# Kernel optimization log

Measured on AMD Instinct MI355X. Metric: run time of the kernel, lower is better.

## Reference

```python
import jax, jax.numpy as jnp
import numpy as np

B, L, DIM = 16, 1024, 768
HEADS, DIM_HEAD = 12, 64
INNER = HEADS * DIM_HEAD  # 768


def _make_perm(key, l, dim):
    # first `dim` entries identity, rest a random permutation of [dim, l*dim)
    tail = dim + jax.random.permutation(key, (l - 1) * dim)
    return jnp.concatenate([jnp.arange(dim), tail]).astype(jnp.int32)


def setup_inputs() -> dict:
    key = jax.random.key(0)
    kx, kq, kk, kv, ko, kp1, kp2 = jax.random.split(key, 7)
    s = DIM ** -0.5
    return {
        "x": jax.random.normal(kx, (B, L, DIM), dtype=jnp.float32),
        "Wq": jax.random.normal(kq, (DIM, INNER), dtype=jnp.float32) * s,
        "Wk": jax.random.normal(kk, (DIM, INNER), dtype=jnp.float32) * s,
        "Wv": jax.random.normal(kv, (DIM, INNER), dtype=jnp.float32) * s,
        "Wo": jax.random.normal(ko, (INNER, DIM), dtype=jnp.float32) * (INNER ** -0.5),
        "bo": jnp.zeros((DIM,), dtype=jnp.float32),
        "permq": _make_perm(kp1, L, DIM),
        "permk": _make_perm(kp2, L, DIM),
    }


def reference(x, Wq, Wk, Wv, Wo, bo, permq, permk):
    b, l, d = x.shape
    scale = DIM_HEAD ** -0.5
    flat = x.reshape(b, l * d)
    xq = flat[:, permq].reshape(b, l, d)  # irregular gather across (seq*dim)
    xk = flat[:, permk].reshape(b, l, d)
    # projections + head split: b n (h d) -> b h n d
    q = (xq @ Wq).reshape(b, l, HEADS, DIM_HEAD).transpose(0, 2, 1, 3)
    k = (xk @ Wk).reshape(b, l, HEADS, DIM_HEAD).transpose(0, 2, 1, 3)
    v = (x @ Wv).reshape(b, l, HEADS, DIM_HEAD).transpose(0, 2, 1, 3)
    dots = jnp.einsum('bhnd,bhmd->bhnm', q, k) * scale
    attn = jax.nn.softmax(dots, axis=-1)
    out = jnp.einsum('bhnm,bhmd->bhnd', attn, v)
    out = out.transpose(0, 2, 1, 3).reshape(b, l, INNER)
    return out @ Wo + bo
```

## Files before the change

kernel.cpp:

```cpp
#include <hip/hip_runtime.h>

typedef unsigned short u16;
typedef __attribute__((ext_vector_type(8))) short bf16x8;
typedef __attribute__((ext_vector_type(4))) float f32x4;
typedef __attribute__((ext_vector_type(16))) float f32x16;

#define MFMA16(a, b, c) __builtin_amdgcn_mfma_f32_16x16x32_bf16(a, b, c, 0, 0, 0)
#define MFMA32(a, b, c) __builtin_amdgcn_mfma_f32_32x32x16_bf16(a, b, c, 0, 0, 0)

#if defined(__has_builtin)
# if __has_builtin(__builtin_amdgcn_cvt_pk_bf16_f32)
#  define HAS_CVT_PK 1
# else
#  define HAS_CVT_PK 0
# endif
#else
# define HAS_CVT_PK 0
#endif

__device__ __forceinline__ u16 f2b(float f) {
    union { float f; unsigned int u; } v;
    v.f = f;
    unsigned int u = v.u;
    return (u16)((u + 0x7fffu + ((u >> 16) & 1u)) >> 16);
}

__device__ __forceinline__ unsigned int f2b_pk(float a, float b) {
#if HAS_CVT_PK
    auto r = __builtin_amdgcn_cvt_pk_bf16_f32(a, b);
    unsigned int u;
    __builtin_memcpy(&u, &r, 4);
    return u;
#else
    return (unsigned int)f2b(a) | ((unsigned int)f2b(b) << 16);
#endif
}

__device__ __forceinline__ unsigned int cvtpk_asm(float a, float b) {
    unsigned int r;
    asm("v_cvt_pk_bf16_f32 %0, %1, %2" : "=v"(r) : "v"(a), "v"(b));
    return r;
}

__device__ __forceinline__ void g2l16(const u16* gsrc, u16* ldst) {
    __builtin_amdgcn_global_load_lds(
        (const __attribute__((address_space(1))) void*)gsrc,
        (__attribute__((address_space(3))) void*)ldst,
        16, 0, 0);
}

__global__ __launch_bounds__(256) void prep_weights(
    const float* __restrict__ Wq, const float* __restrict__ Wk,
    const float* __restrict__ Wv, const float* __restrict__ Wo,
    u16* __restrict__ wqt, u16* __restrict__ wkt,
    u16* __restrict__ wvt, u16* __restrict__ wot) {
    int id = blockIdx.x * 256 + threadIdx.x;
    int k = id / 768, n = id % 768;
    int t = n * 768 + k;
    wqt[t] = f2b(Wq[id] * (0.125f * 1.44269504088896340736f));
    wkt[t] = f2b(Wk[id]);
    wvt[t] = f2b(Wv[id]);
    wot[t] = f2b(Wo[id]);
}

__global__ __launch_bounds__(256) void cast_transpose(
    const float* __restrict__ x, u16* __restrict__ xb, u16* __restrict__ xT) {
    __shared__ __attribute__((aligned(16))) u16 T[16 * 1032];
    int t = threadIdx.x;
    int j0 = blockIdx.x * 1024;
#pragma unroll
    for (int b = 0; b < 16; ++b) {
        float4 v = *(const float4*)&x[(size_t)b * 786432 + j0 + 4 * t];
        uint2 o = make_uint2(f2b_pk(v.x, v.y), f2b_pk(v.z, v.w));
        *(uint2*)&T[b * 1032 + 4 * t] = o;
        *(uint2*)&xb[(size_t)b * 786432 + j0 + 4 * t] = o;
    }
    __syncthreads();
#pragma unroll
    for (int p = 0; p < 4; ++p) {
        int jl = t + 256 * p;
        union { u16 u[16]; int4 v[2]; } r;
#pragma unroll
        for (int b = 0; b < 16; ++b) r.u[b] = T[b * 1032 + jl];
        size_t base = (size_t)(j0 + jl) * 16;
        *(int4*)&xT[base] = r.v[0];
        *(int4*)&xT[base + 8] = r.v[1];
    }
}

__global__ __launch_bounds__(256) void gather_rows(
    const u16* __restrict__ xT, const int* __restrict__ permq,
    const int* __restrict__ permk, u16* __restrict__ xqT,
    u16* __restrict__ xkT) {
    int j = blockIdx.x * 256 + threadIdx.x;
    int pq = permq[j], pk = permk[j];
    const int4* sq = (const int4*)&xT[(size_t)pq * 16];
    const int4* sk = (const int4*)&xT[(size_t)pk * 16];
    int4 q0 = sq[0], q1 = sq[1];
    int4 k0 = sk[0], k1 = sk[1];
    int4* dq = (int4*)&xqT[(size_t)j * 16];
    int4* dk = (int4*)&xkT[(size_t)j * 16];
    dq[0] = q0; dq[1] = q1;
    dk[0] = k0; dk[1] = k1;
}

__global__ __launch_bounds__(256) void untranspose(
    const u16* __restrict__ srcQ, const u16* __restrict__ srcK,
    u16* __restrict__ dstQ, u16* __restrict__ dstK) {
    __shared__ u16 T[16 * 1034];
    const u16* src = blockIdx.y ? srcK : srcQ;
    u16* dst = blockIdx.y ? dstK : dstQ;
    int t = threadIdx.x;
    int j0 = blockIdx.x * 1024;
#pragma unroll
    for (int p = 0; p < 8; ++p) {
        int c = p * 256 + t;
        union { u16 u[8]; int4 v; } r;
        r.v = *(const int4*)&src[(size_t)j0 * 16 + c * 8];
        int jl = c >> 1, h = (c & 1) * 8;
#pragma unroll
        for (int w = 0; w < 8; ++w) T[(h + w) * 1034 + jl] = r.u[w];
    }
    __syncthreads();
#pragma unroll
    for (int b = 0; b < 16; ++b) {
        const unsigned int* s = (const unsigned int*)&T[b * 1034 + 4 * t];
        uint2 o = make_uint2(s[0], s[1]);
        *(uint2*)&dst[(size_t)b * 786432 + j0 + 4 * t] = o;
    }
}

__device__ __forceinline__ void gemm_core(
    const u16* __restrict__ A, const u16* __restrict__ Bt,
    u16* __restrict__ Cb, float* __restrict__ Cf,
    const float* __restrict__ bias, int M, int K, int N, int mode) {
    __shared__ __attribute__((aligned(16))) u16 As[128 * 32];
    __shared__ __attribute__((aligned(16))) u16 Bs[128 * 32];
    int tid = threadIdx.x;
    int m0 = blockIdx.y * 128, n0 = blockIdx.x * 128;
    int wave = tid >> 6, lane = tid & 63;
    int lo = lane & 15, quad = lane >> 4;
    int wm = (wave >> 1) * 64, wn = (wave & 1) * 64;
    f32x4 acc[4][4] = {};

    int c0 = wave * 64 + lane;
    int c1 = 256 + c0;
    const u16* pA0 = A + (size_t)(m0 + (c0 >> 2)) * K + (c0 & 3) * 8;
    const u16* pA1 = A + (size_t)(m0 + (c1 >> 2)) * K + (c1 & 3) * 8;
    const u16* pB0 = Bt + (size_t)(n0 + (c0 >> 2)) * K + (c0 & 3) * 8;
    const u16* pB1 = Bt + (size_t)(n0 + (c1 >> 2)) * K + (c1 & 3) * 8;
    u16* lA0 = &As[(wave * 64) * 8];
    u16* lA1 = &As[(256 + wave * 64) * 8];
    u16* lB0 = &Bs[(wave * 64) * 8];
    u16* lB1 = &Bs[(256 + wave * 64) * 8];

    for (int k0 = 0; k0 < K; k0 += 32) {
        __syncthreads();
        g2l16(pA0, lA0); g2l16(pA1, lA1);
        g2l16(pB0, lB0); g2l16(pB1, lB1);
        pA0 += 32; pA1 += 32; pB0 += 32; pB1 += 32;
        __syncthreads();
        bf16x8 af[4], bf[4];
#pragma unroll
        for (int mi = 0; mi < 4; ++mi)
            af[mi] = *(const bf16x8*)&As[(wm + mi * 16 + lo) * 32 + quad * 8];
#pragma unroll
        for (int nj = 0; nj < 4; ++nj)
            bf[nj] = *(const bf16x8*)&Bs[(wn + nj * 16 + lo) * 32 + quad * 8];
#pragma unroll
        for (int mi = 0; mi < 4; ++mi)
#pragma unroll
            for (int nj = 0; nj < 4; ++nj)
                acc[mi][nj] = MFMA16(af[mi], bf[nj], acc[mi][nj]);
    }
#pragma unroll
    for (int mi = 0; mi < 4; ++mi)
#pragma unroll
        for (int nj = 0; nj < 4; ++nj) {
            int col = n0 + wn + nj * 16 + lo;
#pragma unroll
            for (int r = 0; r < 4; ++r) {
                int row = m0 + wm + mi * 16 + quad * 4 + r;
                float v = acc[mi][nj][r];
                if (mode) Cf[(size_t)row * N + col] = v + bias[col];
                else      Cb[(size_t)row * N + col] = f2b(v);
            }
        }
}

__global__ __launch_bounds__(256) void gemm_qkv(
    const u16* __restrict__ xqb, const u16* __restrict__ wqt, u16* __restrict__ Qb,
    const u16* __restrict__ xkb, const u16* __restrict__ wkt, u16* __restrict__ Kb,
    const u16* __restrict__ xb,  const u16* __restrict__ wvt, u16* __restrict__ Vb) {
    int z = blockIdx.z;
    const u16* A = (z == 0) ? xqb : (z == 1) ? xkb : xb;
    const u16* W = (z == 0) ? wqt : (z == 1) ? wkt : wvt;
    u16* C = (z == 0) ? Qb : (z == 1) ? Kb : Vb;
    gemm_core(A, W, C, nullptr, nullptr, 16384, 768, 768, 0);
}

__global__ __launch_bounds__(256) void gemm_out(
    const u16* __restrict__ A, const u16* __restrict__ Bt,
    float* __restrict__ Cf, const float* __restrict__ bias) {
    gemm_core(A, Bt, nullptr, Cf, bias, 16384, 768, 768, 1);
}

#define LDA 72
__global__ __launch_bounds__(256) void transpose_v(
    const u16* __restrict__ Vb, u16* __restrict__ Vt) {
    __shared__ __attribute__((aligned(16))) u16 tile[64 * LDA];
    int lt = blockIdx.x;
    int bh = blockIdx.y;
    int b = bh / 12, h = bh % 12;
    int tid = threadIdx.x;
    int row = tid >> 3, co = (tid & 7) * 8;
#pragma unroll
    for (int p = 0; p < 2; ++p) {
        int r2 = row + p * 32;
        *(int4*)&tile[r2 * LDA + co] =
            *(const int4*)&Vb[(size_t)(b * 1024 + lt * 64 + r2) * 768 + h * 64 + co];
    }
    __syncthreads();
    int d = tid >> 2, nc = (tid & 3) * 16;
    union { u16 u[16]; int4 v[2]; } tt;
#pragma unroll
    for (int j = 0; j < 16; ++j)
        tt.u[j] = tile[(nc + j) * LDA + d];
    size_t base = ((size_t)bh * 64 + d) * 1024 + lt * 64 + nc;
    *(int4*)&Vt[base] = tt.v[0];
    *(int4*)&Vt[base + 8] = tt.v[1];
}

#define LDK 72
__global__ __launch_bounds__(256) void flash_attn(
    const u16* __restrict__ Qb, const u16* __restrict__ Kb,
    const u16* __restrict__ Vt, u16* __restrict__ AO) {
    __shared__ __attribute__((aligned(16))) u16 Ks[64 * LDK];
    __shared__ __attribute__((aligned(16))) u16 Vs[64 * LDK];
    int id = blockIdx.x;
    int bh = (id & 7) + ((id >> 6) << 3);
    int qt = (id >> 3) & 7;
    int b = bh / 12, h = bh % 12;
    int tid = threadIdx.x, wave = tid >> 6, lane = tid & 63;
    int ln = lane & 31, hi = lane >> 5;
    int q0 = qt * 128;

    bf16x8 qa[4];
    {
        const u16* qrow = &Qb[(size_t)(b * 1024 + q0 + wave * 32 + ln) * 768 + h * 64 + hi * 8];
#pragma unroll
        for (int kk = 0; kk < 4; ++kk)
            qa[kk] = *(const bf16x8*)&qrow[kk * 16];
    }

    const float M2 = 24.0f;
    float l_own = 0.0f;
    f32x16 acc_o[2] = {};
    const size_t kbase = (size_t)b * 1024 * 768 + h * 64;
    const size_t vbase = (size_t)bh * 64 * 1024;
    int srow = tid >> 3, sco = (tid & 7) * 8;

    int4 kr0 = *(const int4*)&Kb[kbase + (size_t)srow * 768 + sco];
    int4 kr1 = *(const int4*)&Kb[kbase + (size_t)(srow + 32) * 768 + sco];
    int4 vr0 = *(const int4*)&Vt[vbase + (size_t)srow * 1024 + sco];
    int4 vr1 = *(const int4*)&Vt[vbase + (size_t)(srow + 32) * 1024 + sco];

    for (int t = 0; t < 16; ++t) {
        __syncthreads();
        *(int4*)&Ks[srow * LDK + sco] = kr0;
        *(int4*)&Ks[(srow + 32) * LDK + sco] = kr1;
        *(int4*)&Vs[srow * LDK + sco] = vr0;
        *(int4*)&Vs[(srow + 32) * LDK + sco] = vr1;
        __syncthreads();
        int tn = (t + 1) & 15;
        kr0 = *(const int4*)&Kb[kbase + (size_t)(tn * 64 + srow) * 768 + sco];
        kr1 = *(const int4*)&Kb[kbase + (size_t)(tn * 64 + srow + 32) * 768 + sco];
        vr0 = *(const int4*)&Vt[vbase + (size_t)srow * 1024 + tn * 64 + sco];
        vr1 = *(const int4*)&Vt[vbase + (size_t)(srow + 32) * 1024 + tn * 64 + sco];
        f32x16 sacc[2] = {};
#pragma unroll
        for (int nj = 0; nj < 2; ++nj)
#pragma unroll
            for (int kk = 0; kk < 4; ++kk) {
                bf16x8 kb = *(const bf16x8*)&Ks[(ln + 32 * nj) * LDK + kk * 16 + hi * 8];
                sacc[nj] = MFMA32(kb, qa[kk], sacc[nj]);
            }
#pragma unroll
        for (int nj = 0; nj < 2; ++nj) {
            float p[16];
#pragma unroll
            for (int r = 0; r < 16; ++r)
                p[r] = __builtin_amdgcn_exp2f(sacc[nj][r] - M2);
            l_own += (((p[0] + p[1]) + (p[2] + p[3])) + ((p[4] + p[5]) + (p[6] + p[7])))
                   + (((p[8] + p[9]) + (p[10] + p[11])) + ((p[12] + p[13]) + (p[14] + p[15])));
            unsigned int c[8];
#pragma unroll
            for (int m = 0; m < 8; ++m)
                c[m] = cvtpk_asm(p[2 * m], p[2 * m + 1]);
            asm("v_permlane32_swap_b32 %0, %1" : "+v"(c[0]), "+v"(c[2]));
            asm("v_permlane32_swap_b32 %0, %1" : "+v"(c[1]), "+v"(c[3]));
            asm("v_permlane32_swap_b32 %0, %1" : "+v"(c[4]), "+v"(c[6]));
            asm("v_permlane32_swap_b32 %0, %1" : "+v"(c[5]), "+v"(c[7]));
            union { unsigned int w[4]; bf16x8 v; } pa0, pa1;
            pa0.w[0] = c[0]; pa0.w[1] = c[1]; pa0.w[2] = c[2]; pa0.w[3] = c[3];
            pa1.w[0] = c[4]; pa1.w[1] = c[5]; pa1.w[2] = c[6]; pa1.w[3] = c[7];
#pragma unroll
            for (int njd = 0; njd < 2; ++njd) {
                bf16x8 vb0 = *(const bf16x8*)&Vs[(ln + 32 * njd) * LDK + (2 * nj) * 16 + hi * 8];
                acc_o[njd] = MFMA32(pa0.v, vb0, acc_o[njd]);
            }
#pragma unroll
            for (int njd = 0; njd < 2; ++njd) {
                bf16x8 vb1 = *(const bf16x8*)&Vs[(ln + 32 * njd) * LDK + (2 * nj + 1) * 16 + hi * 8];
                acc_o[njd] = MFMA32(pa1.v, vb1, acc_o[njd]);
            }
        }
    }
    float l = l_own + __shfl_xor(l_own, 32, 64);
    float inv = 1.0f / l;
#pragma unroll
    for (int r = 0; r < 16; ++r) {
        int qrow = (r & 3) + 8 * (r >> 2) + 4 * hi;
        float invq = __shfl(inv, qrow, 64);
        int row = b * 1024 + q0 + wave * 32 + qrow;
#pragma unroll
        for (int njd = 0; njd < 2; ++njd)
            AO[(size_t)row * 768 + h * 64 + ln + 32 * njd] = f2b(acc_o[njd][r] * invq);
    }
}

static const size_t SZ_W  = (size_t)768 * 768 * 2;
static const size_t SZ_X  = (size_t)16 * 1024 * 768 * 2;
static const size_t OFF_WQT = 0;
static const size_t OFF_WKT = SZ_W;
static const size_t OFF_WVT = 2 * SZ_W;
static const size_t OFF_WOT = 3 * SZ_W;
static const size_t OFF_XB  = 4 * SZ_W;
static const size_t OFF_XQB = OFF_XB  + SZ_X;
static const size_t OFF_XKB = OFF_XQB + SZ_X;
static const size_t OFF_QB  = OFF_XKB + SZ_X;
static const size_t OFF_KB  = OFF_QB  + SZ_X;
static const size_t OFF_VB  = OFF_KB  + SZ_X;
static const size_t OFF_XT  = OFF_QB;
static const size_t OFF_XQT = OFF_KB;
static const size_t OFF_XKT = OFF_VB;
static const size_t OFF_VT  = OFF_XQB;
static const size_t OFF_AO  = OFF_XKB;

extern "C" void kernel_launch(void* const* d_in, const int* in_sizes, int n_in,
                              void* d_out, int out_size, void* d_ws, size_t ws_size,
                              hipStream_t stream) {
    const float* x  = (const float*)d_in[0];
    const float* Wq = (const float*)d_in[1];
    const float* Wk = (const float*)d_in[2];
    const float* Wv = (const float*)d_in[3];
    const float* Wo = (const float*)d_in[4];
    const float* bo = (const float*)d_in[5];
    const int* permq = (const int*)d_in[6];
    const int* permk = (const int*)d_in[7];
    float* out = (float*)d_out;
    char* ws = (char*)d_ws;
    u16* wqt = (u16*)(ws + OFF_WQT);
    u16* wkt = (u16*)(ws + OFF_WKT);
    u16* wvt = (u16*)(ws + OFF_WVT);
    u16* wot = (u16*)(ws + OFF_WOT);
    u16* xb  = (u16*)(ws + OFF_XB);
    u16* xqb = (u16*)(ws + OFF_XQB);
    u16* xkb = (u16*)(ws + OFF_XKB);
    u16* Qb  = (u16*)(ws + OFF_QB);
    u16* Kb  = (u16*)(ws + OFF_KB);
    u16* Vb  = (u16*)(ws + OFF_VB);
    u16* xT  = (u16*)(ws + OFF_XT);
    u16* xqT = (u16*)(ws + OFF_XQT);
    u16* xkT = (u16*)(ws + OFF_XKT);
    u16* Vt  = (u16*)(ws + OFF_VT);
    u16* AO  = (u16*)(ws + OFF_AO);

    prep_weights<<<2304, 256, 0, stream>>>(Wq, Wk, Wv, Wo, wqt, wkt, wvt, wot);
    cast_transpose<<<768, 256, 0, stream>>>(x, xb, xT);
    gather_rows<<<3072, 256, 0, stream>>>(xT, permq, permk, xqT, xkT);
    untranspose<<<dim3(768, 2), 256, 0, stream>>>(xqT, xkT, xqb, xkb);
    gemm_qkv<<<dim3(6, 128, 3), 256, 0, stream>>>(xqb, wqt, Qb, xkb, wkt, Kb, xb, wvt, Vb);
    transpose_v<<<dim3(16, 192), 256, 0, stream>>>(Vb, Vt);
    flash_attn<<<1536, 256, 0, stream>>>(Qb, Kb, Vt, AO);
    gemm_out<<<dim3(6, 128), 256, 0, stream>>>(AO, wot, out, bo);
}
```

Measured before the change: 391.8 us.

## Deepen GEMM K-tile to 64 with XOR-swizzled LDS and XCD-aware block mapping

The shared GEMM core now stages 64-wide K slices instead of 32, which halves the number of barrier-separated load phases. The LDS layout uses an XOR swizzle on 16-byte chunks to avoid bank conflicts on the fragment reads. The QKV and output GEMM launches are flattened to 1D grids and remapped so that consecutive blocks landing on the same XCD share an A row-block, aiming for better L2 reuse. In exchange, LDS use per block doubles, which may lower occupancy.

```diff
diff --git a/kernel.cpp b/kernel.cpp
--- a/kernel.cpp
+++ b/kernel.cpp
@@ -133,45 +133,58 @@
 __device__ __forceinline__ void gemm_core(
     const u16* __restrict__ A, const u16* __restrict__ Bt,
     u16* __restrict__ Cb, float* __restrict__ Cf,
-    const float* __restrict__ bias, int M, int K, int N, int mode) {
-    __shared__ __attribute__((aligned(16))) u16 As[128 * 32];
-    __shared__ __attribute__((aligned(16))) u16 Bs[128 * 32];
+    const float* __restrict__ bias, int m0, int n0, int K, int N, int mode) {
+    __shared__ __attribute__((aligned(16))) u16 As[128 * 64];
+    __shared__ __attribute__((aligned(16))) u16 Bs[128 * 64];
     int tid = threadIdx.x;
-    int m0 = blockIdx.y * 128, n0 = blockIdx.x * 128;
     int wave = tid >> 6, lane = tid & 63;
     int lo = lane & 15, quad = lane >> 4;
     int wm = (wave >> 1) * 64, wn = (wave & 1) * 64;
     f32x4 acc[4][4] = {};
 
-    int c0 = wave * 64 + lane;
-    int c1 = 256 + c0;
-    const u16* pA0 = A + (size_t)(m0 + (c0 >> 2)) * K + (c0 & 3) * 8;
-    const u16* pA1 = A + (size_t)(m0 + (c1 >> 2)) * K + (c1 & 3) * 8;
-    const u16* pB0 = Bt + (size_t)(n0 + (c0 >> 2)) * K + (c0 & 3) * 8;
-    const u16* pB1 = Bt + (size_t)(n0 + (c1 >> 2)) * K + (c1 & 3) * 8;
-    u16* lA0 = &As[(wave * 64) * 8];
-    u16* lA1 = &As[(256 + wave * 64) * 8];
-    u16* lB0 = &Bs[(wave * 64) * 8];
-    u16* lB1 = &Bs[(256 + wave * 64) * 8];
-
-    for (int k0 = 0; k0 < K; k0 += 32) {
+    const u16* pA[4];
+    const u16* pB[4];
+    u16* lA[4];
+    u16* lB[4];
+#pragma unroll
+    for (int p = 0; p < 4; ++p) {
+        int c = p * 256 + wave * 64 + lane;
+        int row = c >> 3;
+        int scol = ((c & 7) ^ (row & 7)) * 8;
+        pA[p] = A + (size_t)(m0 + row) * K + scol;
+        pB[p] = Bt + (size_t)(n0 + row) * K + scol;
+        lA[p] = &As[(p * 256 + wave * 64) * 8];
+        lB[p] = &Bs[(p * 256 + wave * 64) * 8];
+    }
+
+    for (int k0 = 0; k0 < K; k0 += 64) {
         __syncthreads();
-        g2l16(pA0, lA0); g2l16(pA1, lA1);
-        g2l16(pB0, lB0); g2l16(pB1, lB1);
-        pA0 += 32; pA1 += 32; pB0 += 32; pB1 += 32;
+#pragma unroll
+        for (int p = 0; p < 4; ++p) g2l16(pA[p], lA[p]);
+#pragma unroll
+        for (int p = 0; p < 4; ++p) g2l16(pB[p], lB[p]);
+#pragma unroll
+        for (int p = 0; p < 4; ++p) { pA[p] += 64; pB[p] += 64; }
         __syncthreads();
-        bf16x8 af[4], bf[4];
-#pragma unroll
-        for (int mi = 0; mi < 4; ++mi)
-            af[mi] = *(const bf16x8*)&As[(wm + mi * 16 + lo) * 32 + quad * 8];
-#pragma unroll
-        for (int nj = 0; nj < 4; ++nj)
-            bf[nj] = *(const bf16x8*)&Bs[(wn + nj * 16 + lo) * 32 + quad * 8];
-#pragma unroll
-        for (int mi = 0; mi < 4; ++mi)
-#pragma unroll
-            for (int nj = 0; nj < 4; ++nj)
-                acc[mi][nj] = MFMA16(af[mi], bf[nj], acc[mi][nj]);
+#pragma unroll
+        for (int kk = 0; kk < 2; ++kk) {
+            bf16x8 af[4], bf[4];
+#pragma unroll
+            for (int mi = 0; mi < 4; ++mi) {
+                int row = wm + mi * 16 + lo;
+                af[mi] = *(const bf16x8*)&As[row * 64 + (((kk << 2) | quad) ^ (lo & 7)) * 8];
+            }
+#pragma unroll
+            for (int nj = 0; nj < 4; ++nj) {
+                int row = wn + nj * 16 + lo;
+                bf[nj] = *(const bf16x8*)&Bs[row * 64 + (((kk << 2) | quad) ^ (lo & 7)) * 8];
+            }
+#pragma unroll
+            for (int mi = 0; mi < 4; ++mi)
+#pragma unroll
+                for (int nj = 0; nj < 4; ++nj)
+                    acc[mi][nj] = MFMA16(af[mi], bf[nj], acc[mi][nj]);
+        }
     }
 #pragma unroll
     for (int mi = 0; mi < 4; ++mi)
@@ -192,17 +205,25 @@
     const u16* __restrict__ xqb, const u16* __restrict__ wqt, u16* __restrict__ Qb,
     const u16* __restrict__ xkb, const u16* __restrict__ wkt, u16* __restrict__ Kb,
     const u16* __restrict__ xb,  const u16* __restrict__ wvt, u16* __restrict__ Vb) {
-    int z = blockIdx.z;
+    int id = blockIdx.x;
+    int xcd = id & 7, slot = id >> 3;
+    int gi = slot / 6, j = slot % 6;
+    int group = xcd + 8 * gi;
+    int my = group & 127, z = group >> 7;
     const u16* A = (z == 0) ? xqb : (z == 1) ? xkb : xb;
     const u16* W = (z == 0) ? wqt : (z == 1) ? wkt : wvt;
     u16* C = (z == 0) ? Qb : (z == 1) ? Kb : Vb;
-    gemm_core(A, W, C, nullptr, nullptr, 16384, 768, 768, 0);
+    gemm_core(A, W, C, nullptr, nullptr, my * 128, j * 128, 768, 768, 0);
 }
 
 __global__ __launch_bounds__(256) void gemm_out(
     const u16* __restrict__ A, const u16* __restrict__ Bt,
     float* __restrict__ Cf, const float* __restrict__ bias) {
-    gemm_core(A, Bt, nullptr, Cf, bias, 16384, 768, 768, 1);
+    int id = blockIdx.x;
+    int xcd = id & 7, slot = id >> 3;
+    int gi = slot / 6, j = slot % 6;
+    int group = xcd + 8 * gi;
+    gemm_core(A, Bt, nullptr, Cf, bias, group * 128, j * 128, 768, 768, 1);
 }
 
 #define LDA 72
@@ -380,8 +401,8 @@
     cast_transpose<<<768, 256, 0, stream>>>(x, xb, xT);
     gather_rows<<<3072, 256, 0, stream>>>(xT, permq, permk, xqT, xkT);
     untranspose<<<dim3(768, 2), 256, 0, stream>>>(xqT, xkT, xqb, xkb);
-    gemm_qkv<<<dim3(6, 128, 3), 256, 0, stream>>>(xqb, wqt, Qb, xkb, wkt, Kb, xb, wvt, Vb);
+    gemm_qkv<<<2304, 256, 0, stream>>>(xqb, wqt, Qb, xkb, wkt, Kb, xb, wvt, Vb);
     transpose_v<<<dim3(16, 192), 256, 0, stream>>>(Vb, Vt);
     flash_attn<<<1536, 256, 0, stream>>>(Qb, Kb, Vt, AO);
-    gemm_out<<<dim3(6, 128), 256, 0, stream>>>(AO, wot, out, bo);
-}
+    gemm_out<<<768, 256, 0, stream>>>(AO, wot, out, bo);
+}
```

New measurement: 377.4 us. 3.7% less time.
